# Kernel optimization log

Hardware: AMD Instinct MI355X
Metric: run time of the kernel (lower is better)

The kernel has to match this reference:

```python
import jax, jax.numpy as jnp
import numpy as np

EPS = 1e-15


def gmm_conv(x, edge_index, edge_attr, g, mu, sigma, root_w, bias):
    # PyG GMMConv (separate_gaussians=False, aggr='mean', root_weight=True)
    N = x.shape[0]
    K, D = mu.shape          # kernel_size, pseudo-coord dim
    M = bias.shape[0]        # out channels
    src, dst = edge_index[0], edge_index[1]
    xg = (x @ g).reshape(N, K, M)            # [N, K, M] transformed source feats
    x_j = xg[src]                            # [E, K, M] gather
    diff = edge_attr[:, None, :] - mu[None]  # [E, K, D]
    gauss = jnp.exp(jnp.sum(-0.5 * diff * diff / (EPS + sigma[None] ** 2), axis=-1))  # [E, K]
    msg = jnp.sum(x_j * gauss[:, :, None], axis=1)          # [E, M]
    agg = jax.ops.segment_sum(msg, dst, num_segments=N)     # scatter-sum
    cnt = jax.ops.segment_sum(jnp.ones((msg.shape[0], 1), msg.dtype), dst, num_segments=N)
    out = agg / jnp.maximum(cnt, 1.0)                        # scatter-mean (0 for isolated nodes)
    return out + x @ root_w + bias


def setup_inputs() -> dict:
    key = jax.random.key(0)
    ks = jax.random.split(key, 16)
    N, E, D, K = 100000, 1600000, 8, 1
    F_in, H, F_out = 32, 32, 32
    inp = {
        "edge_index": jax.random.randint(ks[0], (2, E), 0, N, dtype=jnp.int64)
        if jax.config.jax_enable_x64 else jax.random.randint(ks[0], (2, E), 0, N).astype(jnp.int32),
        "edge_weight": jax.random.normal(ks[1], (E, D), dtype=jnp.float32),
        "x": jax.random.normal(ks[2], (N, F_in), dtype=jnp.float32),
        # layer 1 params
        "g1": jax.random.normal(ks[3], (F_in, K * H), dtype=jnp.float32) * (1.0 / np.sqrt(F_in)),
        "mu1": jax.random.normal(ks[4], (K, D), dtype=jnp.float32),
        "sigma1": jnp.ones((K, D), dtype=jnp.float32),
        "root1": jax.random.normal(ks[5], (F_in, H), dtype=jnp.float32) * (1.0 / np.sqrt(F_in)),
        "b1": jnp.zeros((H,), dtype=jnp.float32),
        # layer 2 params
        "g2": jax.random.normal(ks[6], (H, K * F_out), dtype=jnp.float32) * (1.0 / np.sqrt(H)),
        "mu2": jax.random.normal(ks[7], (K, D), dtype=jnp.float32),
        "sigma2": jnp.ones((K, D), dtype=jnp.float32),
        "root2": jax.random.normal(ks[8], (H, F_out), dtype=jnp.float32) * (1.0 / np.sqrt(H)),
        "b2": jnp.zeros((F_out,), dtype=jnp.float32),
    }
    return inp


def reference(edge_index, edge_weight, x, g1, mu1, sigma1, root1, b1, g2, mu2, sigma2, root2, b2):
    h = gmm_conv(x, edge_index, edge_weight, g1, mu1, sigma1, root1, b1)
    out = gmm_conv(h, edge_index, edge_weight, g2, mu2, sigma2, root2, b2)
    return out
```

## Files before the change

kernel.cpp:

```cpp
#include <hip/hip_runtime.h>

#define F 32
#define D 8
#define BKN 256
#define BKSH 8
#define EPT 8
#define CAP 4608

typedef unsigned uv2 __attribute__((ext_vector_type(2)));
typedef float fv2 __attribute__((ext_vector_type(2)));
typedef float fv4 __attribute__((ext_vector_type(4)));

__device__ __forceinline__ unsigned f2bf(float f) {
    unsigned u = __float_as_uint(f);
    return (u + 0x7fffu + ((u >> 16) & 1u)) >> 16;
}
__device__ __forceinline__ float bf2f(unsigned b) {
    return __uint_as_float(b << 16);
}

__global__ void build_kernel(const int* __restrict__ ei, const float* __restrict__ ew,
                             const float* __restrict__ mu1, const float* __restrict__ sg1,
                             const float* __restrict__ mu2, const float* __restrict__ sg2,
                             int* __restrict__ bcur, uv2* __restrict__ bin, int NB, int E,
                             const float* __restrict__ x, const float* __restrict__ g1,
                             const float* __restrict__ root1, const float* __restrict__ b1,
                             unsigned short* __restrict__ xgh, float* __restrict__ xr,
                             int N, int binBlocks) {
    __shared__ int hist[512];
    __shared__ int cbase[512];
    __shared__ float gs[F * F];
    __shared__ float rs[F * F];
    int t = threadIdx.x;

    if ((int)blockIdx.x < binBlocks) {
        float m1v[D], i1[D], m2v[D], i2[D];
#pragma unroll
        for (int d = 0; d < D; ++d) {
            m1v[d] = mu1[d];
            i1[d] = -0.5f / (1e-15f + sg1[d] * sg1[d]);
            m2v[d] = mu2[d];
            i2[d] = -0.5f / (1e-15f + sg2[d] * sg2[d]);
        }
        if (t < NB) hist[t] = 0;
        __syncthreads();
        int e0 = blockIdx.x * (512 * EPT) + t;
        unsigned pks[EPT], gps[EPT];
        int bks[EPT];
#pragma unroll
        for (int k = 0; k < EPT; ++k) {
            int e = e0 + k * 512;
            bks[k] = -1;
            if (e < E) {
                int src = __builtin_nontemporal_load(&ei[e]);
                int dst = __builtin_nontemporal_load(&ei[E + e]);
                bks[k] = dst >> BKSH;
                pks[k] = (unsigned)src | ((unsigned)(dst & (BKN - 1)) << 20);
                const fv4* ew4 = (const fv4*)(ew + (size_t)e * D);
                fv4 w0 = __builtin_nontemporal_load(ew4);
                fv4 w1 = __builtin_nontemporal_load(ew4 + 1);
                float w[D] = {w0.x, w0.y, w0.z, w0.w, w1.x, w1.y, w1.z, w1.w};
                float s1 = 0.f, s2 = 0.f;
#pragma unroll
                for (int d = 0; d < D; ++d) {
                    float d1 = w[d] - m1v[d];
                    s1 += d1 * d1 * i1[d];
                    float d2 = w[d] - m2v[d];
                    s2 += d2 * d2 * i2[d];
                }
                gps[k] = f2bf(expf(s1)) | (f2bf(expf(s2)) << 16);
                atomicAdd(&hist[bks[k]], 1);
            }
        }
        __syncthreads();
        if (t < NB) {
            int c = hist[t];
            cbase[t] = t * CAP + (c ? atomicAdd(&bcur[t], c) : 0);
        }
        __syncthreads();
        if (t < NB) hist[t] = 0;
        __syncthreads();
#pragma unroll
        for (int k = 0; k < EPT; ++k) {
            if (bks[k] >= 0) {
                int pos = cbase[bks[k]] + atomicAdd(&hist[bks[k]], 1);
                if (pos < (bks[k] + 1) * CAP) {
                    uv2 p;
                    p.x = pks[k];
                    p.y = gps[k];
                    bin[pos] = p;
                }
            }
        }
    } else {
        for (int i = t; i < F * F; i += 512) {
            gs[i] = g1[i];
            rs[i] = root1[i];
        }
        __syncthreads();
        int m = t & 31;
        int node = (int)((((size_t)blockIdx.x - binBlocks) * 512 + t) >> 5);
        if (node >= N) return;
        float xv = x[(size_t)node * F + m];
        int base = t & 32;
        float accg = 0.f, accr = 0.f;
#pragma unroll
        for (int c = 0; c < F; ++c) {
            float xc = __shfl(xv, base + c, 64);
            accg += xc * gs[c * F + m];
            accr += xc * rs[c * F + m];
        }
        xgh[(size_t)node * F + m] = (unsigned short)f2bf(accg);
        xr[(size_t)node * F + m] = accr + b1[m];
    }
}

__global__ void csr_kernel(const uv2* __restrict__ bin, const int* __restrict__ bcur,
                           int2* __restrict__ off2, uv2* __restrict__ edata, int N) {
    int b = blockIdx.x;
    int ebase = b * CAP;
    int nE = min(bcur[b], CAP);
    __shared__ int cnt[BKN];
    __shared__ int cur[BKN];
    __shared__ int ps[BKN];
    int t = threadIdx.x;
    if (t < BKN) cnt[t] = 0;
    __syncthreads();
    for (int i = t; i < nE; i += 1024)
        atomicAdd(&cnt[(bin[ebase + i].x >> 20) & (BKN - 1)], 1);
    __syncthreads();
    int a = (t < BKN) ? cnt[t] : 0;
    if (t < BKN) ps[t] = a;
    __syncthreads();
    for (int d = 1; d < BKN; d <<= 1) {
        int u = (t < BKN && t >= d) ? ps[t - d] : 0;
        __syncthreads();
        if (t < BKN) ps[t] += u;
        __syncthreads();
    }
    if (t < BKN) {
        int excl = ps[t] - a;
        cur[t] = excl;
        int node = (b << BKSH) + t;
        if (node < N) {
            int2 o;
            o.x = ebase + excl;
            o.y = ebase + excl + a;
            off2[node] = o;
        }
    }
    __syncthreads();
    for (int i = t; i < nE; i += 1024) {
        uv2 p = bin[ebase + i];
        int dl = (p.x >> 20) & (BKN - 1);
        int pos = ebase + atomicAdd(&cur[dl], 1);
        uv2 q;
        q.x = p.x & 0xfffffu;
        q.y = p.y;
        edata[pos] = q;
    }
}

__global__ void agg1_fuse_kernel(const int2* __restrict__ off2,
                                 const uv2* __restrict__ edata,
                                 const unsigned* __restrict__ xg32,
                                 const fv2* __restrict__ xr2,
                                 const float* __restrict__ g2,
                                 const float* __restrict__ root2,
                                 const float* __restrict__ b2,
                                 unsigned* __restrict__ xg32_out,
                                 fv2* __restrict__ xr2_out,
                                 int N) {
    __shared__ float gs[F * F];
    __shared__ float rs[F * F];
    for (int i = threadIdx.x; i < F * F; i += blockDim.x) {
        gs[i] = g2[i];
        rs[i] = root2[i];
    }
    __syncthreads();
    int t = threadIdx.x;
    int l = t & 15;
    int node = (int)((blockIdx.x * (size_t)blockDim.x + t) >> 4);
    if (node >= N) return;
    int base = t & 48;
    int2 so = off2[node];
    int s0 = so.x, s1 = so.y;
    int deg = s1 - s0;
    float a0 = 0.f, a1 = 0.f;
    for (int i = s0; i < s1; i += 16) {
        uv2 ed = __builtin_nontemporal_load(&edata[min(i + l, s1 - 1)]);
        bool ok = (i + l < s1);
        unsigned pk = ok ? ed.x : 0u;
        float gv = ok ? bf2f(ed.y & 0xffffu) : 0.f;
        unsigned xv[16];
        float gj[16];
#pragma unroll
        for (int j = 0; j < 16; ++j) {
            unsigned s = __shfl(pk, base + j, 64);
            gj[j] = __shfl(gv, base + j, 64);
            xv[j] = xg32[s * 16 + l];
        }
#pragma unroll
        for (int j = 0; j < 16; ++j) {
            a0 += bf2f(xv[j] & 0xffffu) * gj[j];
            a1 += __uint_as_float(xv[j] & 0xffff0000u) * gj[j];
        }
    }
    float inv = (deg > 0) ? 1.f / (float)deg : 0.f;
    fv2 r = __builtin_nontemporal_load(&xr2[(size_t)node * 16 + l]);
    float hx = a0 * inv + r.x;
    float hy = a1 * inv + r.y;
    float ag0 = 0.f, ag1 = 0.f, ar0 = 0.f, ar1 = 0.f;
#pragma unroll
    for (int c = 0; c < F; ++c) {
        float src = (c & 1) ? hy : hx;
        float hc = __shfl(src, base + (c >> 1), 64);
        ag0 += hc * gs[c * F + 2 * l];
        ag1 += hc * gs[c * F + 2 * l + 1];
        ar0 += hc * rs[c * F + 2 * l];
        ar1 += hc * rs[c * F + 2 * l + 1];
    }
    unsigned og = f2bf(ag0) | (f2bf(ag1) << 16);
    __builtin_nontemporal_store(og, &xg32_out[(size_t)node * 16 + l]);
    fv2 xo;
    xo.x = ar0 + b2[2 * l];
    xo.y = ar1 + b2[2 * l + 1];
    __builtin_nontemporal_store(xo, &xr2_out[(size_t)node * 16 + l]);
}

__global__ void aggregate2_kernel(const int2* __restrict__ off2,
                                  const uv2* __restrict__ edata,
                                  const unsigned* __restrict__ xg32,
                                  const fv2* __restrict__ xr2,
                                  fv2* __restrict__ out2, int N) {
    int t = threadIdx.x;
    int l = t & 15;
    int node = (int)((blockIdx.x * (size_t)blockDim.x + t) >> 4);
    if (node >= N) return;
    int base = t & 48;
    int2 so = off2[node];
    int s0 = so.x, s1 = so.y;
    int deg = s1 - s0;
    float a0 = 0.f, a1 = 0.f;
    for (int i = s0; i < s1; i += 16) {
        uv2 ed = __builtin_nontemporal_load(&edata[min(i + l, s1 - 1)]);
        bool ok = (i + l < s1);
        unsigned pk = ok ? ed.x : 0u;
        float gv = ok ? __uint_as_float(ed.y & 0xffff0000u) : 0.f;
        unsigned xv[16];
        float gj[16];
#pragma unroll
        for (int j = 0; j < 16; ++j) {
            unsigned s = __shfl(pk, base + j, 64);
            gj[j] = __shfl(gv, base + j, 64);
            xv[j] = xg32[s * 16 + l];
        }
#pragma unroll
        for (int j = 0; j < 16; ++j) {
            a0 += bf2f(xv[j] & 0xffffu) * gj[j];
            a1 += __uint_as_float(xv[j] & 0xffff0000u) * gj[j];
        }
    }
    float inv = (deg > 0) ? 1.f / (float)deg : 0.f;
    fv2 r = __builtin_nontemporal_load(&xr2[(size_t)node * 16 + l]);
    fv2 o;
    o.x = a0 * inv + r.x;
    o.y = a1 * inv + r.y;
    __builtin_nontemporal_store(o, &out2[(size_t)node * 16 + l]);
}

extern "C" void kernel_launch(void* const* d_in, const int* in_sizes, int n_in,
                              void* d_out, int out_size, void* d_ws, size_t ws_size,
                              hipStream_t stream) {
    const int*   ei   = (const int*)d_in[0];
    const float* ew   = (const float*)d_in[1];
    const float* x    = (const float*)d_in[2];
    const float* g1   = (const float*)d_in[3];
    const float* mu1  = (const float*)d_in[4];
    const float* sg1  = (const float*)d_in[5];
    const float* r1   = (const float*)d_in[6];
    const float* b1   = (const float*)d_in[7];
    const float* g2   = (const float*)d_in[8];
    const float* mu2  = (const float*)d_in[9];
    const float* sg2  = (const float*)d_in[10];
    const float* r2   = (const float*)d_in[11];
    const float* b2   = (const float*)d_in[12];
    float* out = (float*)d_out;

    const int E = in_sizes[0] / 2;
    const int N = in_sizes[2] / F;
    const size_t NF = (size_t)N * F;
    const int NB = (N + BKN - 1) / BKN;

    uv2*            bin   = (uv2*)d_ws;
    uv2*            edata = bin + (size_t)NB * CAP;
    float*          xr1   = (float*)(edata + (size_t)NB * CAP);
    float*          xr2w  = xr1 + NF;
    unsigned short* xgh1  = (unsigned short*)(xr2w + NF);
    unsigned short* xgh2  = xgh1 + NF;
    int2*           off2  = (int2*)(xgh2 + NF);
    int*            bcur  = (int*)(off2 + N);

    const int BT = 256;
    const int blk_bin = (E + 512 * EPT - 1) / (512 * EPT);
    const int blk_tr  = (int)((NF + 511) / 512);
    const int blk_agg = (int)(((size_t)N * 16 + BT - 1) / BT);

    (void)hipMemsetAsync(bcur, 0, NB * sizeof(int), stream);

    build_kernel<<<blk_bin + blk_tr, 512, 0, stream>>>(
        ei, ew, mu1, sg1, mu2, sg2, bcur, bin, NB, E,
        x, g1, r1, b1, xgh1, xr1, N, blk_bin);

    csr_kernel<<<NB, 1024, 0, stream>>>(bin, bcur, off2, edata, N);

    agg1_fuse_kernel<<<blk_agg, BT, 0, stream>>>(off2, edata, (const unsigned*)xgh1,
                                                 (const fv2*)xr1, g2, r2, b2,
                                                 (unsigned*)xgh2, (fv2*)xr2w, N);

    aggregate2_kernel<<<blk_agg, BT, 0, stream>>>(off2, edata, (const unsigned*)xgh2,
                                                  (const fv2*)xr2w, (fv2*)out, N);
}
```

Baseline: 239.6 us.

## Replace bucketed binning CSR build with degree count, global scan, and atomic scatter

Replaces the two-pass bucket binning (shared-memory histogram into fixed-capacity bins, then per-bucket local sort) with a degree-count pass, a three-kernel global prefix scan, and an edge kernel that scatters each edge directly to its CSR slot using global atomics on per-node cursors. This removes the intermediate bin buffer round-trip and the fixed-capacity overflow cap. In exchange it adds more kernel launches, reads the dst indices twice, and uses 1.6M scattered global atomics plus random-position writes. The edata load in the first aggregation also drops its nontemporal hint.

After: 368.9 us. 1.54x slower.

```diff
diff --git a/kernel.cpp b/kernel.cpp
--- a/kernel.cpp
+++ b/kernel.cpp
@@ -2,10 +2,7 @@
 
 #define F 32
 #define D 8
-#define BKN 256
-#define BKSH 8
 #define EPT 8
-#define CAP 4608
 
 typedef unsigned uv2 __attribute__((ext_vector_type(2)));
 typedef float fv2 __attribute__((ext_vector_type(2)));
@@ -19,77 +16,22 @@
     return __uint_as_float(b << 16);
 }
 
-__global__ void build_kernel(const int* __restrict__ ei, const float* __restrict__ ew,
-                             const float* __restrict__ mu1, const float* __restrict__ sg1,
-                             const float* __restrict__ mu2, const float* __restrict__ sg2,
-                             int* __restrict__ bcur, uv2* __restrict__ bin, int NB, int E,
-                             const float* __restrict__ x, const float* __restrict__ g1,
-                             const float* __restrict__ root1, const float* __restrict__ b1,
-                             unsigned short* __restrict__ xgh, float* __restrict__ xr,
-                             int N, int binBlocks) {
-    __shared__ int hist[512];
-    __shared__ int cbase[512];
+__global__ void pre_kernel(const int* __restrict__ ei, int* __restrict__ deg, int E,
+                           const float* __restrict__ x, const float* __restrict__ g1,
+                           const float* __restrict__ root1, const float* __restrict__ b1,
+                           unsigned short* __restrict__ xgh, float* __restrict__ xr,
+                           int N, int degBlocks) {
     __shared__ float gs[F * F];
     __shared__ float rs[F * F];
     int t = threadIdx.x;
-
-    if ((int)blockIdx.x < binBlocks) {
-        float m1v[D], i1[D], m2v[D], i2[D];
-#pragma unroll
-        for (int d = 0; d < D; ++d) {
-            m1v[d] = mu1[d];
-            i1[d] = -0.5f / (1e-15f + sg1[d] * sg1[d]);
-            m2v[d] = mu2[d];
-            i2[d] = -0.5f / (1e-15f + sg2[d] * sg2[d]);
-        }
-        if (t < NB) hist[t] = 0;
-        __syncthreads();
+    if ((int)blockIdx.x < degBlocks) {
         int e0 = blockIdx.x * (512 * EPT) + t;
-        unsigned pks[EPT], gps[EPT];
-        int bks[EPT];
 #pragma unroll
         for (int k = 0; k < EPT; ++k) {
             int e = e0 + k * 512;
-            bks[k] = -1;
             if (e < E) {
-                int src = __builtin_nontemporal_load(&ei[e]);
                 int dst = __builtin_nontemporal_load(&ei[E + e]);
-                bks[k] = dst >> BKSH;
-                pks[k] = (unsigned)src | ((unsigned)(dst & (BKN - 1)) << 20);
-                const fv4* ew4 = (const fv4*)(ew + (size_t)e * D);
-                fv4 w0 = __builtin_nontemporal_load(ew4);
-                fv4 w1 = __builtin_nontemporal_load(ew4 + 1);
-                float w[D] = {w0.x, w0.y, w0.z, w0.w, w1.x, w1.y, w1.z, w1.w};
-                float s1 = 0.f, s2 = 0.f;
-#pragma unroll
-                for (int d = 0; d < D; ++d) {
-                    float d1 = w[d] - m1v[d];
-                    s1 += d1 * d1 * i1[d];
-                    float d2 = w[d] - m2v[d];
-                    s2 += d2 * d2 * i2[d];
-                }
-                gps[k] = f2bf(expf(s1)) | (f2bf(expf(s2)) << 16);
-                atomicAdd(&hist[bks[k]], 1);
-            }
-        }
-        __syncthreads();
-        if (t < NB) {
-            int c = hist[t];
-            cbase[t] = t * CAP + (c ? atomicAdd(&bcur[t], c) : 0);
-        }
-        __syncthreads();
-        if (t < NB) hist[t] = 0;
-        __syncthreads();
-#pragma unroll
-        for (int k = 0; k < EPT; ++k) {
-            if (bks[k] >= 0) {
-                int pos = cbase[bks[k]] + atomicAdd(&hist[bks[k]], 1);
-                if (pos < (bks[k] + 1) * CAP) {
-                    uv2 p;
-                    p.x = pks[k];
-                    p.y = gps[k];
-                    bin[pos] = p;
-                }
+                atomicAdd(&deg[dst], 1);
             }
         }
     } else {
@@ -99,7 +41,7 @@
         }
         __syncthreads();
         int m = t & 31;
-        int node = (int)((((size_t)blockIdx.x - binBlocks) * 512 + t) >> 5);
+        int node = (int)((((size_t)blockIdx.x - degBlocks) * 512 + t) >> 5);
         if (node >= N) return;
         float xv = x[(size_t)node * F + m];
         int base = t & 32;
@@ -115,49 +57,90 @@
     }
 }
 
-__global__ void csr_kernel(const uv2* __restrict__ bin, const int* __restrict__ bcur,
-                           int2* __restrict__ off2, uv2* __restrict__ edata, int N) {
-    int b = blockIdx.x;
-    int ebase = b * CAP;
-    int nE = min(bcur[b], CAP);
-    __shared__ int cnt[BKN];
-    __shared__ int cur[BKN];
-    __shared__ int ps[BKN];
-    int t = threadIdx.x;
-    if (t < BKN) cnt[t] = 0;
+__global__ void scan1_kernel(const int* __restrict__ deg, int* __restrict__ loc,
+                             int* __restrict__ part, int N) {
+    __shared__ int s[1024];
+    int t = threadIdx.x;
+    int g = blockIdx.x * 1024 + t;
+    int v = (g < N) ? deg[g] : 0;
+    s[t] = v;
     __syncthreads();
-    for (int i = t; i < nE; i += 1024)
-        atomicAdd(&cnt[(bin[ebase + i].x >> 20) & (BKN - 1)], 1);
+    for (int d = 1; d < 1024; d <<= 1) {
+        int u = (t >= d) ? s[t - d] : 0;
+        __syncthreads();
+        s[t] += u;
+        __syncthreads();
+    }
+    if (g < N) loc[g] = s[t] - v;
+    if (t == 1023) part[blockIdx.x] = s[t];
+}
+
+__global__ void scan2_kernel(int* __restrict__ part, int nb) {
+    __shared__ int s[128];
+    int t = threadIdx.x;
+    int v = (t < nb) ? part[t] : 0;
+    s[t] = v;
     __syncthreads();
-    int a = (t < BKN) ? cnt[t] : 0;
-    if (t < BKN) ps[t] = a;
-    __syncthreads();
-    for (int d = 1; d < BKN; d <<= 1) {
-        int u = (t < BKN && t >= d) ? ps[t - d] : 0;
-        __syncthreads();
-        if (t < BKN) ps[t] += u;
-        __syncthreads();
-    }
-    if (t < BKN) {
-        int excl = ps[t] - a;
-        cur[t] = excl;
-        int node = (b << BKSH) + t;
-        if (node < N) {
-            int2 o;
-            o.x = ebase + excl;
-            o.y = ebase + excl + a;
-            off2[node] = o;
-        }
-    }
-    __syncthreads();
-    for (int i = t; i < nE; i += 1024) {
-        uv2 p = bin[ebase + i];
-        int dl = (p.x >> 20) & (BKN - 1);
-        int pos = ebase + atomicAdd(&cur[dl], 1);
-        uv2 q;
-        q.x = p.x & 0xfffffu;
-        q.y = p.y;
-        edata[pos] = q;
+    for (int d = 1; d < 128; d <<= 1) {
+        int u = (t >= d) ? s[t - d] : 0;
+        __syncthreads();
+        s[t] += u;
+        __syncthreads();
+    }
+    if (t < nb) part[t] = s[t] - v;
+}
+
+__global__ void scan3_kernel(const int* __restrict__ loc, const int* __restrict__ part,
+                             const int* __restrict__ deg, int* __restrict__ cur,
+                             int2* __restrict__ off2, int N) {
+    int g = blockIdx.x * 1024 + threadIdx.x;
+    if (g >= N) return;
+    int st = loc[g] + part[blockIdx.x];
+    cur[g] = st;
+    int2 o;
+    o.x = st;
+    o.y = st + deg[g];
+    off2[g] = o;
+}
+
+__global__ void edge_kernel(const int* __restrict__ ei, const float* __restrict__ ew,
+                            const float* __restrict__ mu1, const float* __restrict__ sg1,
+                            const float* __restrict__ mu2, const float* __restrict__ sg2,
+                            int* __restrict__ cur, uv2* __restrict__ edata, int E) {
+    float m1v[D], i1[D], m2v[D], i2[D];
+#pragma unroll
+    for (int d = 0; d < D; ++d) {
+        m1v[d] = mu1[d];
+        i1[d] = -0.5f / (1e-15f + sg1[d] * sg1[d]);
+        m2v[d] = mu2[d];
+        i2[d] = -0.5f / (1e-15f + sg2[d] * sg2[d]);
+    }
+    int t = threadIdx.x;
+    int e0 = blockIdx.x * (512 * EPT) + t;
+#pragma unroll
+    for (int k = 0; k < EPT; ++k) {
+        int e = e0 + k * 512;
+        if (e < E) {
+            int src = __builtin_nontemporal_load(&ei[e]);
+            int dst = __builtin_nontemporal_load(&ei[E + e]);
+            const fv4* ew4 = (const fv4*)(ew + (size_t)e * D);
+            fv4 w0 = __builtin_nontemporal_load(ew4);
+            fv4 w1 = __builtin_nontemporal_load(ew4 + 1);
+            float w[D] = {w0.x, w0.y, w0.z, w0.w, w1.x, w1.y, w1.z, w1.w};
+            float s1 = 0.f, s2 = 0.f;
+#pragma unroll
+            for (int d = 0; d < D; ++d) {
+                float d1 = w[d] - m1v[d];
+                s1 += d1 * d1 * i1[d];
+                float d2 = w[d] - m2v[d];
+                s2 += d2 * d2 * i2[d];
+            }
+            int pos = atomicAdd(&cur[dst], 1);
+            uv2 q;
+            q.x = (unsigned)src;
+            q.y = f2bf(expf(s1)) | (f2bf(expf(s2)) << 16);
+            edata[pos] = q;
+        }
     }
 }
 
@@ -188,7 +171,7 @@
     int deg = s1 - s0;
     float a0 = 0.f, a1 = 0.f;
     for (int i = s0; i < s1; i += 16) {
-        uv2 ed = __builtin_nontemporal_load(&edata[min(i + l, s1 - 1)]);
+        uv2 ed = edata[min(i + l, s1 - 1)];
         bool ok = (i + l < s1);
         unsigned pk = ok ? ed.x : 0u;
         float gv = ok ? bf2f(ed.y & 0xffffu) : 0.f;
@@ -290,29 +273,35 @@
     const int E = in_sizes[0] / 2;
     const int N = in_sizes[2] / F;
     const size_t NF = (size_t)N * F;
-    const int NB = (N + BKN - 1) / BKN;
-
-    uv2*            bin   = (uv2*)d_ws;
-    uv2*            edata = bin + (size_t)NB * CAP;
-    float*          xr1   = (float*)(edata + (size_t)NB * CAP);
+
+    uv2*            edata = (uv2*)d_ws;
+    float*          xr1   = (float*)(edata + (size_t)E);
     float*          xr2w  = xr1 + NF;
     unsigned short* xgh1  = (unsigned short*)(xr2w + NF);
     unsigned short* xgh2  = xgh1 + NF;
     int2*           off2  = (int2*)(xgh2 + NF);
-    int*            bcur  = (int*)(off2 + N);
+    int*            deg   = (int*)(off2 + N);
+    int*            cur   = deg + N;
+    int*            loc   = cur + N;
+    int*            part  = loc + N;
 
     const int BT = 256;
-    const int blk_bin = (E + 512 * EPT - 1) / (512 * EPT);
-    const int blk_tr  = (int)((NF + 511) / 512);
-    const int blk_agg = (int)(((size_t)N * 16 + BT - 1) / BT);
-
-    (void)hipMemsetAsync(bcur, 0, NB * sizeof(int), stream);
-
-    build_kernel<<<blk_bin + blk_tr, 512, 0, stream>>>(
-        ei, ew, mu1, sg1, mu2, sg2, bcur, bin, NB, E,
-        x, g1, r1, b1, xgh1, xr1, N, blk_bin);
-
-    csr_kernel<<<NB, 1024, 0, stream>>>(bin, bcur, off2, edata, N);
+    const int blk_edge = (E + 512 * EPT - 1) / (512 * EPT);
+    const int blk_tr   = (int)((NF + 511) / 512);
+    const int blk_scan = (N + 1023) / 1024;
+    const int blk_agg  = (int)(((size_t)N * 16 + BT - 1) / BT);
+
+    (void)hipMemsetAsync(deg, 0, (size_t)N * sizeof(int), stream);
+
+    pre_kernel<<<blk_edge + blk_tr, 512, 0, stream>>>(
+        ei, deg, E, x, g1, r1, b1, xgh1, xr1, N, blk_edge);
+
+    scan1_kernel<<<blk_scan, 1024, 0, stream>>>(deg, loc, part, N);
+    scan2_kernel<<<1, 128, 0, stream>>>(part, blk_scan);
+    scan3_kernel<<<blk_scan, 1024, 0, stream>>>(loc, part, deg, cur, off2, N);
+
+    edge_kernel<<<blk_edge, 512, 0, stream>>>(ei, ew, mu1, sg1, mu2, sg2,
+                                              cur, edata, E);
 
     agg1_fuse_kernel<<<blk_agg, BT, 0, stream>>>(off2, edata, (const unsigned*)xgh1,
                                                  (const fv2*)xr1, g2, r2, b2,
```
